# Performance work log

Hardware: AMD Instinct MI355X
Metric: run time of the kernel (lower is better)

## Reference

```python
import jax, jax.numpy as jnp
import numpy as np

N_NODES = 50000
N_EDGES = 800000
F_IN, F_LAT, F_OUT = 64, 64, 64


def _graph_conv(x, W, b, src, dst, deg_out_isqrt, deg_in_isqrt):
    # DGL GraphConv, norm='both': D_out^{-1/2} scaling on src side,
    # linear transform (mult-first since in_feats >= out_feats),
    # scatter-sum to dst, D_in^{-1/2} scaling on dst side, + bias.
    n = x.shape[0]
    h = (x * deg_out_isqrt[:, None]) @ W              # [N, F_out]
    msg = h[src]                                      # [E, F_out] gather
    agg = jax.ops.segment_sum(msg, dst, num_segments=n)  # [N, F_out] scatter
    return agg * deg_in_isqrt[:, None] + b


def setup_inputs() -> dict:
    key = jax.random.key(0)
    ks = jax.random.split(key, 6)
    x = jax.random.normal(ks[0], (N_NODES, F_IN), dtype=jnp.float32)
    W1 = jax.random.normal(ks[1], (F_IN, F_LAT), dtype=jnp.float32) / np.sqrt(F_IN)
    b1 = jnp.zeros((F_LAT,), dtype=jnp.float32)
    W2 = jax.random.normal(ks[2], (F_LAT, F_OUT), dtype=jnp.float32) / np.sqrt(F_LAT)
    b2 = jnp.zeros((F_OUT,), dtype=jnp.float32)
    src = jax.random.randint(ks[3], (N_EDGES,), 0, N_NODES, dtype=jnp.int32)
    dst = jax.random.randint(ks[4], (N_EDGES,), 0, N_NODES, dtype=jnp.int32)
    return {"x": x, "W1": W1, "b1": b1, "W2": W2, "b2": b2, "src": src, "dst": dst}


def reference(x, W1, b1, W2, b2, src, dst):
    n = x.shape[0]
    ones = jnp.ones((src.shape[0],), dtype=x.dtype)
    deg_out = jax.ops.segment_sum(ones, src, num_segments=n)
    deg_in = jax.ops.segment_sum(ones, dst, num_segments=n)
    deg_out_isqrt = jnp.where(deg_out > 0, jax.lax.rsqrt(jnp.maximum(deg_out, 1.0)), 0.0)
    deg_in_isqrt = jnp.where(deg_in > 0, jax.lax.rsqrt(jnp.maximum(deg_in, 1.0)), 0.0)
    h = _graph_conv(x, W1, b1, src, dst, deg_out_isqrt, deg_in_isqrt)
    h = jax.nn.relu(h)
    out = _graph_conv(h, W2, b2, src, dst, deg_out_isqrt, deg_in_isqrt)
    return out
```

## Files before the change

kernel.cpp:

```cpp
#include <hip/hip_runtime.h>

#define NF 64
#define BC 32
#define RANGE 16384
#define RWORDS (RANGE / 4)
#define RANGE2 16384
#define PSPLIT 4

typedef __attribute__((ext_vector_type(8))) short short8;
typedef __attribute__((ext_vector_type(4))) float floatx4;

__device__ __forceinline__ unsigned short f2bf(float f) {
  unsigned int u = __float_as_uint(f);
  return (unsigned short)((u + 0x7fffu + ((u >> 16) & 1u)) >> 16);
}

__global__ __launch_bounds__(512) void hist_kernel(
    const int* __restrict__ src, const int* __restrict__ dst,
    unsigned char* __restrict__ Gout, unsigned char* __restrict__ Gin,
    unsigned char* __restrict__ rank, int n, int nE, int R, int chunk) {
  __shared__ int cnt[RWORDS];
  const int rb = blockIdx.x % (R * BC);
  const int kind = blockIdx.x / (R * BC);
  const int r = rb / BC, b = rb % BC;
  const int r0 = r * RANGE;
  for (int i = threadIdx.x; i < RWORDS; i += 512) cnt[i] = 0;
  __syncthreads();
  const int lo = b * chunk, hi = min(lo + chunk, nE);
  const int* keys = kind ? src : dst;
  const int n4 = (hi > lo) ? ((hi - lo) >> 2) : 0;
  const int4* keys4 = (const int4*)(keys + lo);
  if (kind == 0) {
    for (int i = threadIdx.x; i < n4; i += 512) {
      int4 v = keys4[i];
      int e0 = lo + 4 * i;
      unsigned int k, old, sh;
      k = (unsigned int)(v.x - r0);
      if (k < (unsigned int)RANGE) { sh = (k & 3) * 8; old = atomicAdd(&cnt[k >> 2], 1u << sh); rank[e0 + 0] = (unsigned char)(old >> sh); }
      k = (unsigned int)(v.y - r0);
      if (k < (unsigned int)RANGE) { sh = (k & 3) * 8; old = atomicAdd(&cnt[k >> 2], 1u << sh); rank[e0 + 1] = (unsigned char)(old >> sh); }
      k = (unsigned int)(v.z - r0);
      if (k < (unsigned int)RANGE) { sh = (k & 3) * 8; old = atomicAdd(&cnt[k >> 2], 1u << sh); rank[e0 + 2] = (unsigned char)(old >> sh); }
      k = (unsigned int)(v.w - r0);
      if (k < (unsigned int)RANGE) { sh = (k & 3) * 8; old = atomicAdd(&cnt[k >> 2], 1u << sh); rank[e0 + 3] = (unsigned char)(old >> sh); }
    }
    for (int e = lo + 4 * n4 + threadIdx.x; e < hi; e += 512) {
      unsigned int k = (unsigned int)(keys[e] - r0);
      if (k < (unsigned int)RANGE) {
        unsigned int sh = (k & 3) * 8;
        unsigned int old = atomicAdd(&cnt[k >> 2], 1u << sh);
        rank[e] = (unsigned char)(old >> sh);
      }
    }
    __syncthreads();
    unsigned int* Gw = (unsigned int*)(Gin + (size_t)b * n + r0);
    for (int i = threadIdx.x; i < RWORDS; i += 512)
      if (r0 + 4 * i < n) Gw[i] = (unsigned int)cnt[i];
  } else {
    for (int i = threadIdx.x; i < n4; i += 512) {
      int4 v = keys4[i];
      unsigned int k;
      k = (unsigned int)(v.x - r0);
      if (k < (unsigned int)RANGE) atomicAdd(&cnt[k >> 2], 1u << ((k & 3) * 8));
      k = (unsigned int)(v.y - r0);
      if (k < (unsigned int)RANGE) atomicAdd(&cnt[k >> 2], 1u << ((k & 3) * 8));
      k = (unsigned int)(v.z - r0);
      if (k < (unsigned int)RANGE) atomicAdd(&cnt[k >> 2], 1u << ((k & 3) * 8));
      k = (unsigned int)(v.w - r0);
      if (k < (unsigned int)RANGE) atomicAdd(&cnt[k >> 2], 1u << ((k & 3) * 8));
    }
    for (int e = lo + 4 * n4 + threadIdx.x; e < hi; e += 512) {
      unsigned int k = (unsigned int)(keys[e] - r0);
      if (k < (unsigned int)RANGE) atomicAdd(&cnt[k >> 2], 1u << ((k & 3) * 8));
    }
    __syncthreads();
    unsigned int* Gw = (unsigned int*)(Gout + (size_t)b * n + r0);
    for (int i = threadIdx.x; i < RWORDS; i += 512)
      if (r0 + 4 * i < n) Gw[i] = (unsigned int)cnt[i];
  }
}

__global__ __launch_bounds__(256) void colscan_scan1_kernel(
    unsigned char* __restrict__ Gin, const unsigned char* __restrict__ Gout,
    float* __restrict__ so, float* __restrict__ si,
    int* __restrict__ lscan, int* __restrict__ bsum, int n) {
  __shared__ int s[256];
  const int tid = threadIdx.x;
  const int i = blockIdx.x * 256 + tid;
  int di = 0;
  if (i < n) {
    int base = 0;
    #pragma unroll 8
    for (int b = 0; b < BC; ++b) {
      int c = Gin[(size_t)b * n + i];
      Gin[(size_t)b * n + i] = (unsigned char)base;
      base += c;
    }
    di = base;
    int dsum = 0;
    #pragma unroll 8
    for (int b = 0; b < BC; ++b) dsum += Gout[(size_t)b * n + i];
    si[i] = di > 0 ? rsqrtf((float)di) : 0.f;
    so[i] = dsum > 0 ? rsqrtf((float)dsum) : 0.f;
  }
  s[tid] = di;
  __syncthreads();
  #pragma unroll
  for (int off = 1; off < 256; off <<= 1) {
    int t2 = (tid >= off) ? s[tid - off] : 0;
    __syncthreads();
    s[tid] += t2;
    __syncthreads();
  }
  if (i < n) lscan[i] = s[tid] - di;
  if (tid == 255) bsum[blockIdx.x] = s[255];
}

__global__ __launch_bounds__(256) void scan3_kernel(
    const int* __restrict__ lscan, const int* __restrict__ bsum,
    int* __restrict__ row_start, int n, int nE) {
  __shared__ int red[256];
  const int tid = threadIdx.x;
  const int b = blockIdx.x;
  red[tid] = (tid < b) ? bsum[tid] : 0;
  __syncthreads();
  #pragma unroll
  for (int s = 128; s > 0; s >>= 1) {
    if (tid < s) red[tid] += red[tid + s];
    __syncthreads();
  }
  const int off = red[0];
  const int i = b * 256 + tid;
  if (b == 0 && tid == 0) row_start[n] = nE;
  if (i < n) row_start[i] = lscan[i] + off;
}

__device__ __forceinline__ void mfma_gemm_core(
    const unsigned short* __restrict__ Ab, const unsigned short* __restrict__ Wt,
    unsigned short* __restrict__ H, int row0, int n, int t) {
  const int w = t >> 6, lane = t & 63;
  const int quad = lane >> 4, l15 = lane & 15;
  const short8 a0 = *(const short8*)&Ab[(w * 16 + l15) * 72 + quad * 8];
  const short8 a1 = *(const short8*)&Ab[(w * 16 + l15) * 72 + 32 + quad * 8];
  #pragma unroll
  for (int cg = 0; cg < 4; ++cg) {
    const short8 b0 = *(const short8*)&Wt[(cg * 16 + l15) * 72 + quad * 8];
    const short8 b1 = *(const short8*)&Wt[(cg * 16 + l15) * 72 + 32 + quad * 8];
    floatx4 acc = {0.f, 0.f, 0.f, 0.f};
    acc = __builtin_amdgcn_mfma_f32_16x16x32_bf16(a0, b0, acc, 0, 0, 0);
    acc = __builtin_amdgcn_mfma_f32_16x16x32_bf16(a1, b1, acc, 0, 0, 0);
    #pragma unroll
    for (int reg = 0; reg < 4; ++reg) {
      int grow = row0 + w * 16 + quad * 4 + reg;
      if (grow < n) H[(size_t)grow * NF + cg * 16 + l15] = f2bf(acc[reg]);
    }
  }
}

__device__ __forceinline__ void stage_wt512(
    const float* __restrict__ W, unsigned short* __restrict__ Wt, int t) {
  #pragma unroll
  for (int i = 0; i < 8; ++i) {
    int idx = t + 512 * i;
    int k = idx >> 6, j = idx & 63;
    Wt[j * 72 + k] = f2bf(W[idx]);
  }
}

__global__ __launch_bounds__(512) void place_gemm1_kernel(
    const float* __restrict__ A, const float* __restrict__ so,
    const float* __restrict__ W, unsigned short* __restrict__ H, int n, int ggrid,
    const int* __restrict__ src, const int* __restrict__ dst,
    const unsigned char* __restrict__ rank, const int* __restrict__ row_start,
    const unsigned char* __restrict__ Gin,
    unsigned short* __restrict__ sorted, int nE, int chunk) {
  __shared__ __align__(16) char smem[RANGE2 * 4];
  const int t = threadIdx.x;
  if ((int)blockIdx.x >= ggrid) {
    int* posb = (int*)smem;
    const int pb = blockIdx.x - ggrid;
    const int r = pb / (BC * PSPLIT);
    const int rem = pb % (BC * PSPLIT);
    const int b = rem / PSPLIT;
    const int s = rem % PSPLIT;
    const int r0 = r * RANGE2;
    const int lim = min(RANGE2, n - r0);
    {
      const int4* rs4 = (const int4*)(row_start + r0);
      const unsigned int* g4 = (const unsigned int*)(Gin + (size_t)b * n + r0);
      int4* posb4 = (int4*)posb;
      const int lim4 = lim >> 2;
      for (int i = t; i < lim4; i += 512) {
        int4 rs = rs4[i];
        unsigned int gg = g4[i];
        int4 o;
        o.x = rs.x + (int)(gg & 0xffu);
        o.y = rs.y + (int)((gg >> 8) & 0xffu);
        o.z = rs.z + (int)((gg >> 16) & 0xffu);
        o.w = rs.w + (int)(gg >> 24);
        posb4[i] = o;
      }
    }
    __syncthreads();
    const int lo = b * chunk, hi = min(lo + chunk, nE);
    const int n4 = (hi > lo) ? ((hi - lo) >> 2) : 0;
    const int4* dst4 = (const int4*)(dst + lo);
    const int4* src4 = (const int4*)(src + lo);
    const unsigned int* rank4 = (const unsigned int*)(rank + lo);
    for (int i = t + s * 512; i < n4; i += 512 * PSPLIT) {
      int4 dv = dst4[i];
      int4 sv = src4[i];
      unsigned int rv = rank4[i];
      unsigned int k;
      k = (unsigned int)(dv.x - r0);
      if (k < (unsigned int)lim) sorted[posb[k] + (int)(rv & 0xffu)] = (unsigned short)sv.x;
      k = (unsigned int)(dv.y - r0);
      if (k < (unsigned int)lim) sorted[posb[k] + (int)((rv >> 8) & 0xffu)] = (unsigned short)sv.y;
      k = (unsigned int)(dv.z - r0);
      if (k < (unsigned int)lim) sorted[posb[k] + (int)((rv >> 16) & 0xffu)] = (unsigned short)sv.z;
      k = (unsigned int)(dv.w - r0);
      if (k < (unsigned int)lim) sorted[posb[k] + (int)(rv >> 24)] = (unsigned short)sv.w;
    }
    if (s == 0) {
      for (int e = lo + 4 * n4 + t; e < hi; e += 512) {
        unsigned int k = (unsigned int)(dst[e] - r0);
        if (k < (unsigned int)lim)
          sorted[posb[k] + (int)rank[e]] = (unsigned short)src[e];
      }
    }
    return;
  }
  unsigned short* Ab = (unsigned short*)smem;
  unsigned short* Wt = (unsigned short*)(smem + 128 * 72 * 2);
  stage_wt512(W, Wt, t);
  const int row0 = blockIdx.x * 128;
  #pragma unroll
  for (int i = 0; i < 4; ++i) {
    int idx = t + 512 * i;
    int r = idx >> 4, c4 = idx & 15;
    int gr = row0 + r;
    float4 v = {0.f, 0.f, 0.f, 0.f};
    float sc = 0.f;
    if (gr < n) {
      v = *(const float4*)&A[(size_t)gr * NF + c4 * 4];
      sc = so[gr];
    }
    ushort4 o;
    o.x = f2bf(v.x * sc); o.y = f2bf(v.y * sc);
    o.z = f2bf(v.z * sc); o.w = f2bf(v.w * sc);
    *(ushort4*)&Ab[r * 72 + c4 * 4] = o;
  }
  __syncthreads();
  const int wid = t >> 6;
  const int half = wid >> 2;
  mfma_gemm_core(Ab + half * 64 * 72, Wt, H, row0 + half * 64, n,
                 (wid & 3) * 64 + (t & 63));
}

__device__ __forceinline__ void gather_sum(
    const unsigned short* __restrict__ H, const unsigned short* __restrict__ srcs,
    int beg, int end, int g, int c, float* acc) {
  const float4* Hv = (const float4*)H;
  int e = beg;
  for (; e + 16 <= end; e += 16) {
    int ia = srcs[e + g];
    int ib = srcs[e + 8 + g];
    float4 va = Hv[(size_t)ia * 8 + c];
    float4 vb = Hv[(size_t)ib * 8 + c];
    const unsigned int* pa = (const unsigned int*)&va;
    const unsigned int* pb = (const unsigned int*)&vb;
    #pragma unroll
    for (int k = 0; k < 4; ++k) {
      acc[2 * k]     += __uint_as_float(pa[k] << 16) + __uint_as_float(pb[k] << 16);
      acc[2 * k + 1] += __uint_as_float(pa[k] & 0xffff0000u) + __uint_as_float(pb[k] & 0xffff0000u);
    }
  }
  if (e + 8 <= end) {
    int ia = srcs[e + g];
    float4 va = Hv[(size_t)ia * 8 + c];
    const unsigned int* pa = (const unsigned int*)&va;
    #pragma unroll
    for (int k = 0; k < 4; ++k) {
      acc[2 * k]     += __uint_as_float(pa[k] << 16);
      acc[2 * k + 1] += __uint_as_float(pa[k] & 0xffff0000u);
    }
    e += 8;
  }
  if (e < end) {
    int idx = (e + g < end) ? (e + g) : (end - 1);
    float m = (e + g < end) ? 1.f : 0.f;
    int ia = srcs[idx];
    float4 va = Hv[(size_t)ia * 8 + c];
    const unsigned int* pa = (const unsigned int*)&va;
    #pragma unroll
    for (int k = 0; k < 4; ++k) {
      acc[2 * k]     += m * __uint_as_float(pa[k] << 16);
      acc[2 * k + 1] += m * __uint_as_float(pa[k] & 0xffff0000u);
    }
  }
  #pragma unroll
  for (int d = 8; d <= 32; d <<= 1) {
    #pragma unroll
    for (int k = 0; k < 8; ++k) acc[k] += __shfl_xor(acc[k], d);
  }
}

__global__ __launch_bounds__(256) void agg1_kernel(
    const unsigned short* __restrict__ H1, const int* __restrict__ row_start,
    const unsigned short* __restrict__ srcs, const float* __restrict__ si,
    const float* __restrict__ so, const float* __restrict__ b1,
    unsigned short* __restrict__ T, int n) {
  int node = blockIdx.x * 4 + (threadIdx.x >> 6);
  if (node >= n) return;
  const int lane = threadIdx.x & 63;
  const int g = lane >> 3;
  const int c = lane & 7;
  float acc[8] = {0, 0, 0, 0, 0, 0, 0, 0};
  gather_sum(H1, srcs, row_start[node], row_start[node + 1], g, c, acc);
  if (g == 0) {
    const float sin = si[node];
    const float son = so[node];
    ushort4 o0, o1;
    float v;
    v = fmaxf(fmaf(acc[0], sin, b1[c * 8 + 0]), 0.f) * son; o0.x = f2bf(v);
    v = fmaxf(fmaf(acc[1], sin, b1[c * 8 + 1]), 0.f) * son; o0.y = f2bf(v);
    v = fmaxf(fmaf(acc[2], sin, b1[c * 8 + 2]), 0.f) * son; o0.z = f2bf(v);
    v = fmaxf(fmaf(acc[3], sin, b1[c * 8 + 3]), 0.f) * son; o0.w = f2bf(v);
    v = fmaxf(fmaf(acc[4], sin, b1[c * 8 + 4]), 0.f) * son; o1.x = f2bf(v);
    v = fmaxf(fmaf(acc[5], sin, b1[c * 8 + 5]), 0.f) * son; o1.y = f2bf(v);
    v = fmaxf(fmaf(acc[6], sin, b1[c * 8 + 6]), 0.f) * son; o1.z = f2bf(v);
    v = fmaxf(fmaf(acc[7], sin, b1[c * 8 + 7]), 0.f) * son; o1.w = f2bf(v);
    *(ushort4*)&T[(size_t)node * NF + c * 8]     = o0;
    *(ushort4*)&T[(size_t)node * NF + c * 8 + 4] = o1;
  }
}

__global__ __launch_bounds__(256) void agg2_kernel(
    const unsigned short* __restrict__ Tb, const int* __restrict__ row_start,
    const unsigned short* __restrict__ srcs, const float* __restrict__ si,
    const float* __restrict__ W2, const float* __restrict__ b2,
    float* __restrict__ out, int n) {
  __shared__ __align__(16) float W2s[64 * 64];
  __shared__ float u[4][64];
  const int t = threadIdx.x;
  #pragma unroll
  for (int i = 0; i < 4; ++i)
    *(float4*)&W2s[t * 4 + 1024 * i] = *(const float4*)&W2[t * 4 + 1024 * i];
  const int w = t >> 6;
  const int lane = t & 63;
  const int g = lane >> 3;
  const int c = lane & 7;
  const int node = blockIdx.x * 4 + w;
  const bool valid = node < n;
  float acc[8] = {0, 0, 0, 0, 0, 0, 0, 0};
  if (valid) gather_sum(Tb, srcs, row_start[node], row_start[node + 1], g, c, acc);
  if (g == 0) {
    const float sin = valid ? si[node] : 0.f;
    #pragma unroll
    for (int k = 0; k < 8; ++k) u[w][c * 8 + k] = acc[k] * sin;
  }
  __syncthreads();
  if (valid) {
    float r = b2[lane];
    #pragma unroll
    for (int k = 0; k < 64; ++k) r = fmaf(u[w][k], W2s[k * 64 + lane], r);
    out[(size_t)node * NF + lane] = r;
  }
}

extern "C" void kernel_launch(void* const* d_in, const int* in_sizes, int n_in,
                              void* d_out, int out_size, void* d_ws, size_t ws_size,
                              hipStream_t stream) {
  const float* x  = (const float*)d_in[0];
  const float* W1 = (const float*)d_in[1];
  const float* b1 = (const float*)d_in[2];
  const float* W2 = (const float*)d_in[3];
  const float* b2 = (const float*)d_in[4];
  const int* src  = (const int*)d_in[5];
  const int* dst  = (const int*)d_in[6];
  float* out = (float*)d_out;

  const int N = in_sizes[0] / NF;
  const int E = in_sizes[5];
  const int NB = (N + 255) / 256;
  const int R  = (N + RANGE - 1) / RANGE;
  const int R2 = (N + RANGE2 - 1) / RANGE2;
  const int CH = (((E + BC - 1) / BC) + 3) & ~3;
  (void)ws_size;

  char* ws = (char*)d_ws;
  size_t p = 0;
  auto alloc = [&](size_t bytes) -> void* {
    void* r = ws + p;
    p = (p + bytes + 255) & ~(size_t)255;
    return r;
  };
  float* so         = (float*)alloc((size_t)N * 4);
  float* si         = (float*)alloc((size_t)N * 4);
  int*   row_start  = (int*)  alloc((size_t)(N + 1) * 4);
  int*   bsum       = (int*)  alloc((size_t)NB * 4);
  int*   lscan      = (int*)  alloc((size_t)N * 4);
  unsigned short* sorted_u16 = (unsigned short*)alloc((size_t)E * 2);
  unsigned char*  rank  = (unsigned char*)alloc((size_t)E);
  unsigned short* h1    = (unsigned short*)alloc((size_t)N * NF * 2);
  unsigned char*  G_in  = (unsigned char*)alloc((size_t)BC * N);
  unsigned char*  G_out = (unsigned char*)alloc((size_t)BC * N);
  unsigned short* tb    = (unsigned short*)alloc((size_t)N * NF * 2);

  hist_kernel<<<2 * R * BC, 512, 0, stream>>>(src, dst, G_out, G_in, rank,
                                              N, E, R, CH);

  colscan_scan1_kernel<<<NB, 256, 0, stream>>>(G_in, G_out, so, si,
                                               lscan, bsum, N);

  scan3_kernel<<<NB, 256, 0, stream>>>(lscan, bsum, row_start, N, E);

  const int ggrid = (N + 127) / 128;
  const int pgrid = R2 * BC * PSPLIT;
  const int agrid = (N + 3) / 4;

  place_gemm1_kernel<<<ggrid + pgrid, 512, 0, stream>>>(
      x, so, W1, h1, N, ggrid, src, dst, rank, row_start, G_in,
      sorted_u16, E, CH);

  agg1_kernel<<<agrid, 256, 0, stream>>>(h1, row_start, sorted_u16, si, so, b1, tb, N);

  agg2_kernel<<<agrid, 256, 0, stream>>>(tb, row_start, sorted_u16, si, W2, b2, out, N);
}
```

Baseline: 169.6 us.

## Drop rank array, fuse scan into place, move GEMM1 into aggregation

```diff
diff --git a/kernel.cpp b/kernel.cpp
--- a/kernel.cpp
+++ b/kernel.cpp
@@ -1,14 +1,12 @@
 #include <hip/hip_runtime.h>
 
 #define NF 64
-#define BC 32
+#define BC 64
 #define RANGE 16384
 #define RWORDS (RANGE / 4)
 #define RANGE2 16384
-#define PSPLIT 4
 
 typedef __attribute__((ext_vector_type(8))) short short8;
-typedef __attribute__((ext_vector_type(4))) float floatx4;
 
 __device__ __forceinline__ unsigned short f2bf(float f) {
   unsigned int u = __float_as_uint(f);
@@ -18,7 +16,7 @@
 __global__ __launch_bounds__(512) void hist_kernel(
     const int* __restrict__ src, const int* __restrict__ dst,
     unsigned char* __restrict__ Gout, unsigned char* __restrict__ Gin,
-    unsigned char* __restrict__ rank, int n, int nE, int R, int chunk) {
+    int n, int nE, int R, int chunk) {
   __shared__ int cnt[RWORDS];
   const int rb = blockIdx.x % (R * BC);
   const int kind = blockIdx.x / (R * BC);
@@ -30,64 +28,40 @@
   const int* keys = kind ? src : dst;
   const int n4 = (hi > lo) ? ((hi - lo) >> 2) : 0;
   const int4* keys4 = (const int4*)(keys + lo);
-  if (kind == 0) {
-    for (int i = threadIdx.x; i < n4; i += 512) {
-      int4 v = keys4[i];
-      int e0 = lo + 4 * i;
-      unsigned int k, old, sh;
-      k = (unsigned int)(v.x - r0);
-      if (k < (unsigned int)RANGE) { sh = (k & 3) * 8; old = atomicAdd(&cnt[k >> 2], 1u << sh); rank[e0 + 0] = (unsigned char)(old >> sh); }
-      k = (unsigned int)(v.y - r0);
-      if (k < (unsigned int)RANGE) { sh = (k & 3) * 8; old = atomicAdd(&cnt[k >> 2], 1u << sh); rank[e0 + 1] = (unsigned char)(old >> sh); }
-      k = (unsigned int)(v.z - r0);
-      if (k < (unsigned int)RANGE) { sh = (k & 3) * 8; old = atomicAdd(&cnt[k >> 2], 1u << sh); rank[e0 + 2] = (unsigned char)(old >> sh); }
-      k = (unsigned int)(v.w - r0);
-      if (k < (unsigned int)RANGE) { sh = (k & 3) * 8; old = atomicAdd(&cnt[k >> 2], 1u << sh); rank[e0 + 3] = (unsigned char)(old >> sh); }
-    }
-    for (int e = lo + 4 * n4 + threadIdx.x; e < hi; e += 512) {
-      unsigned int k = (unsigned int)(keys[e] - r0);
-      if (k < (unsigned int)RANGE) {
-        unsigned int sh = (k & 3) * 8;
-        unsigned int old = atomicAdd(&cnt[k >> 2], 1u << sh);
-        rank[e] = (unsigned char)(old >> sh);
-      }
-    }
-    __syncthreads();
-    unsigned int* Gw = (unsigned int*)(Gin + (size_t)b * n + r0);
-    for (int i = threadIdx.x; i < RWORDS; i += 512)
-      if (r0 + 4 * i < n) Gw[i] = (unsigned int)cnt[i];
-  } else {
-    for (int i = threadIdx.x; i < n4; i += 512) {
-      int4 v = keys4[i];
-      unsigned int k;
-      k = (unsigned int)(v.x - r0);
-      if (k < (unsigned int)RANGE) atomicAdd(&cnt[k >> 2], 1u << ((k & 3) * 8));
-      k = (unsigned int)(v.y - r0);
-      if (k < (unsigned int)RANGE) atomicAdd(&cnt[k >> 2], 1u << ((k & 3) * 8));
-      k = (unsigned int)(v.z - r0);
-      if (k < (unsigned int)RANGE) atomicAdd(&cnt[k >> 2], 1u << ((k & 3) * 8));
-      k = (unsigned int)(v.w - r0);
-      if (k < (unsigned int)RANGE) atomicAdd(&cnt[k >> 2], 1u << ((k & 3) * 8));
-    }
-    for (int e = lo + 4 * n4 + threadIdx.x; e < hi; e += 512) {
-      unsigned int k = (unsigned int)(keys[e] - r0);
-      if (k < (unsigned int)RANGE) atomicAdd(&cnt[k >> 2], 1u << ((k & 3) * 8));
-    }
-    __syncthreads();
-    unsigned int* Gw = (unsigned int*)(Gout + (size_t)b * n + r0);
-    for (int i = threadIdx.x; i < RWORDS; i += 512)
-      if (r0 + 4 * i < n) Gw[i] = (unsigned int)cnt[i];
-  }
-}
-
-__global__ __launch_bounds__(256) void colscan_scan1_kernel(
+  for (int i = threadIdx.x; i < n4; i += 512) {
+    int4 v = keys4[i];
+    unsigned int k;
+    k = (unsigned int)(v.x - r0);
+    if (k < (unsigned int)RANGE) atomicAdd(&cnt[k >> 2], 1u << ((k & 3) * 8));
+    k = (unsigned int)(v.y - r0);
+    if (k < (unsigned int)RANGE) atomicAdd(&cnt[k >> 2], 1u << ((k & 3) * 8));
+    k = (unsigned int)(v.z - r0);
+    if (k < (unsigned int)RANGE) atomicAdd(&cnt[k >> 2], 1u << ((k & 3) * 8));
+    k = (unsigned int)(v.w - r0);
+    if (k < (unsigned int)RANGE) atomicAdd(&cnt[k >> 2], 1u << ((k & 3) * 8));
+  }
+  for (int e = lo + 4 * n4 + threadIdx.x; e < hi; e += 512) {
+    unsigned int k = (unsigned int)(keys[e] - r0);
+    if (k < (unsigned int)RANGE) atomicAdd(&cnt[k >> 2], 1u << ((k & 3) * 8));
+  }
+  __syncthreads();
+  unsigned char* G = kind ? Gout : Gin;
+  unsigned int* Gw = (unsigned int*)(G + (size_t)b * n + r0);
+  for (int i = threadIdx.x; i < RWORDS; i += 512)
+    if (r0 + 4 * i < n) Gw[i] = (unsigned int)cnt[i];
+}
+
+__global__ __launch_bounds__(256) void colscan_kernel(
     unsigned char* __restrict__ Gin, const unsigned char* __restrict__ Gout,
+    const float* __restrict__ x, unsigned short* __restrict__ xb,
     float* __restrict__ so, float* __restrict__ si,
     int* __restrict__ lscan, int* __restrict__ bsum, int n) {
   __shared__ int s[256];
+  __shared__ float sos[256];
   const int tid = threadIdx.x;
   const int i = blockIdx.x * 256 + tid;
   int di = 0;
+  float so_v = 0.f;
   if (i < n) {
     int base = 0;
     #pragma unroll 8
@@ -101,8 +75,10 @@
     #pragma unroll 8
     for (int b = 0; b < BC; ++b) dsum += Gout[(size_t)b * n + i];
     si[i] = di > 0 ? rsqrtf((float)di) : 0.f;
-    so[i] = dsum > 0 ? rsqrtf((float)dsum) : 0.f;
-  }
+    so_v = dsum > 0 ? rsqrtf((float)dsum) : 0.f;
+    so[i] = so_v;
+  }
+  sos[tid] = so_v;
   s[tid] = di;
   __syncthreads();
   #pragma unroll
@@ -114,147 +90,92 @@
   }
   if (i < n) lscan[i] = s[tid] - di;
   if (tid == 255) bsum[blockIdx.x] = s[255];
-}
-
-__global__ __launch_bounds__(256) void scan3_kernel(
+  const size_t base4 = (size_t)blockIdx.x * 256 * (NF / 4);
+  const float4* xv = (const float4*)x;
+  #pragma unroll
+  for (int j = 0; j < 16; ++j) {
+    int ci = tid + 256 * j;
+    int nl = ci >> 4;
+    if (blockIdx.x * 256 + nl < n) {
+      float4 v = xv[base4 + ci];
+      float sc = sos[nl];
+      ushort4 o;
+      o.x = f2bf(v.x * sc); o.y = f2bf(v.y * sc);
+      o.z = f2bf(v.z * sc); o.w = f2bf(v.w * sc);
+      *(ushort4*)&xb[(base4 + ci) * 4] = o;
+    }
+  }
+}
+
+__global__ __launch_bounds__(512) void place_kernel(
+    const int* __restrict__ src, const int* __restrict__ dst,
     const int* __restrict__ lscan, const int* __restrict__ bsum,
-    int* __restrict__ row_start, int n, int nE) {
-  __shared__ int red[256];
-  const int tid = threadIdx.x;
-  const int b = blockIdx.x;
-  red[tid] = (tid < b) ? bsum[tid] : 0;
-  __syncthreads();
-  #pragma unroll
-  for (int s = 128; s > 0; s >>= 1) {
-    if (tid < s) red[tid] += red[tid + s];
+    const unsigned char* __restrict__ Gin, int* __restrict__ row_start,
+    unsigned short* __restrict__ sorted, int n, int nE, int nb, int chunk) {
+  __shared__ int posb[RANGE2];
+  __shared__ int offs[256];
+  const int t = threadIdx.x;
+  const int r = blockIdx.x / BC, b = blockIdx.x % BC;
+  const int r0 = r * RANGE2;
+  const int lim = min(RANGE2, n - r0);
+  if (t < 256) offs[t] = (t < nb) ? bsum[t] : 0;
+  __syncthreads();
+  #pragma unroll
+  for (int off = 1; off < 256; off <<= 1) {
+    int v = 0;
+    if (t < 256 && t >= off) v = offs[t - off];
     __syncthreads();
-  }
-  const int off = red[0];
-  const int i = b * 256 + tid;
-  if (b == 0 && tid == 0) row_start[n] = nE;
-  if (i < n) row_start[i] = lscan[i] + off;
-}
-
-__device__ __forceinline__ void mfma_gemm_core(
-    const unsigned short* __restrict__ Ab, const unsigned short* __restrict__ Wt,
-    unsigned short* __restrict__ H, int row0, int n, int t) {
-  const int w = t >> 6, lane = t & 63;
-  const int quad = lane >> 4, l15 = lane & 15;
-  const short8 a0 = *(const short8*)&Ab[(w * 16 + l15) * 72 + quad * 8];
-  const short8 a1 = *(const short8*)&Ab[(w * 16 + l15) * 72 + 32 + quad * 8];
-  #pragma unroll
-  for (int cg = 0; cg < 4; ++cg) {
-    const short8 b0 = *(const short8*)&Wt[(cg * 16 + l15) * 72 + quad * 8];
-    const short8 b1 = *(const short8*)&Wt[(cg * 16 + l15) * 72 + 32 + quad * 8];
-    floatx4 acc = {0.f, 0.f, 0.f, 0.f};
-    acc = __builtin_amdgcn_mfma_f32_16x16x32_bf16(a0, b0, acc, 0, 0, 0);
-    acc = __builtin_amdgcn_mfma_f32_16x16x32_bf16(a1, b1, acc, 0, 0, 0);
-    #pragma unroll
-    for (int reg = 0; reg < 4; ++reg) {
-      int grow = row0 + w * 16 + quad * 4 + reg;
-      if (grow < n) H[(size_t)grow * NF + cg * 16 + l15] = f2bf(acc[reg]);
-    }
-  }
-}
-
-__device__ __forceinline__ void stage_wt512(
-    const float* __restrict__ W, unsigned short* __restrict__ Wt, int t) {
-  #pragma unroll
-  for (int i = 0; i < 8; ++i) {
-    int idx = t + 512 * i;
-    int k = idx >> 6, j = idx & 63;
-    Wt[j * 72 + k] = f2bf(W[idx]);
-  }
-}
-
-__global__ __launch_bounds__(512) void place_gemm1_kernel(
-    const float* __restrict__ A, const float* __restrict__ so,
-    const float* __restrict__ W, unsigned short* __restrict__ H, int n, int ggrid,
-    const int* __restrict__ src, const int* __restrict__ dst,
-    const unsigned char* __restrict__ rank, const int* __restrict__ row_start,
-    const unsigned char* __restrict__ Gin,
-    unsigned short* __restrict__ sorted, int nE, int chunk) {
-  __shared__ __align__(16) char smem[RANGE2 * 4];
-  const int t = threadIdx.x;
-  if ((int)blockIdx.x >= ggrid) {
-    int* posb = (int*)smem;
-    const int pb = blockIdx.x - ggrid;
-    const int r = pb / (BC * PSPLIT);
-    const int rem = pb % (BC * PSPLIT);
-    const int b = rem / PSPLIT;
-    const int s = rem % PSPLIT;
-    const int r0 = r * RANGE2;
-    const int lim = min(RANGE2, n - r0);
-    {
-      const int4* rs4 = (const int4*)(row_start + r0);
-      const unsigned int* g4 = (const unsigned int*)(Gin + (size_t)b * n + r0);
-      int4* posb4 = (int4*)posb;
-      const int lim4 = lim >> 2;
-      for (int i = t; i < lim4; i += 512) {
-        int4 rs = rs4[i];
-        unsigned int gg = g4[i];
-        int4 o;
-        o.x = rs.x + (int)(gg & 0xffu);
-        o.y = rs.y + (int)((gg >> 8) & 0xffu);
-        o.z = rs.z + (int)((gg >> 16) & 0xffu);
-        o.w = rs.w + (int)(gg >> 24);
-        posb4[i] = o;
-      }
-    }
+    if (t < 256) offs[t] += v;
     __syncthreads();
-    const int lo = b * chunk, hi = min(lo + chunk, nE);
-    const int n4 = (hi > lo) ? ((hi - lo) >> 2) : 0;
-    const int4* dst4 = (const int4*)(dst + lo);
-    const int4* src4 = (const int4*)(src + lo);
-    const unsigned int* rank4 = (const unsigned int*)(rank + lo);
-    for (int i = t + s * 512; i < n4; i += 512 * PSPLIT) {
-      int4 dv = dst4[i];
-      int4 sv = src4[i];
-      unsigned int rv = rank4[i];
-      unsigned int k;
-      k = (unsigned int)(dv.x - r0);
-      if (k < (unsigned int)lim) sorted[posb[k] + (int)(rv & 0xffu)] = (unsigned short)sv.x;
-      k = (unsigned int)(dv.y - r0);
-      if (k < (unsigned int)lim) sorted[posb[k] + (int)((rv >> 8) & 0xffu)] = (unsigned short)sv.y;
-      k = (unsigned int)(dv.z - r0);
-      if (k < (unsigned int)lim) sorted[posb[k] + (int)((rv >> 16) & 0xffu)] = (unsigned short)sv.z;
-      k = (unsigned int)(dv.w - r0);
-      if (k < (unsigned int)lim) sorted[posb[k] + (int)(rv >> 24)] = (unsigned short)sv.w;
-    }
-    if (s == 0) {
-      for (int e = lo + 4 * n4 + t; e < hi; e += 512) {
-        unsigned int k = (unsigned int)(dst[e] - r0);
-        if (k < (unsigned int)lim)
-          sorted[posb[k] + (int)rank[e]] = (unsigned short)src[e];
-      }
-    }
-    return;
-  }
-  unsigned short* Ab = (unsigned short*)smem;
-  unsigned short* Wt = (unsigned short*)(smem + 128 * 72 * 2);
-  stage_wt512(W, Wt, t);
-  const int row0 = blockIdx.x * 128;
-  #pragma unroll
-  for (int i = 0; i < 4; ++i) {
-    int idx = t + 512 * i;
-    int r = idx >> 4, c4 = idx & 15;
-    int gr = row0 + r;
-    float4 v = {0.f, 0.f, 0.f, 0.f};
-    float sc = 0.f;
-    if (gr < n) {
-      v = *(const float4*)&A[(size_t)gr * NF + c4 * 4];
-      sc = so[gr];
-    }
-    ushort4 o;
-    o.x = f2bf(v.x * sc); o.y = f2bf(v.y * sc);
-    o.z = f2bf(v.z * sc); o.w = f2bf(v.w * sc);
-    *(ushort4*)&Ab[r * 72 + c4 * 4] = o;
-  }
-  __syncthreads();
-  const int wid = t >> 6;
-  const int half = wid >> 2;
-  mfma_gemm_core(Ab + half * 64 * 72, Wt, H, row0 + half * 64, n,
-                 (wid & 3) * 64 + (t & 63));
+  }
+  {
+    const int4* ls4 = (const int4*)(lscan + r0);
+    const unsigned int* g4 = (const unsigned int*)(Gin + (size_t)b * n + r0);
+    const int lim4 = lim >> 2;
+    for (int i = t; i < lim4; i += 512) {
+      int gi0 = r0 + 4 * i;
+      int j = gi0 >> 8;
+      int off = (j > 0) ? offs[j - 1] : 0;
+      int4 ls = ls4[i];
+      unsigned int gg = g4[i];
+      int4 rs;
+      rs.x = ls.x + off; rs.y = ls.y + off;
+      rs.z = ls.z + off; rs.w = ls.w + off;
+      int4 o;
+      o.x = rs.x + (int)(gg & 0xffu);
+      o.y = rs.y + (int)((gg >> 8) & 0xffu);
+      o.z = rs.z + (int)((gg >> 16) & 0xffu);
+      o.w = rs.w + (int)(gg >> 24);
+      *(int4*)&posb[4 * i] = o;
+      if (b == 0) *(int4*)&row_start[gi0] = rs;
+    }
+  }
+  if (b == 0 && r == 0 && t == 0) row_start[n] = nE;
+  __syncthreads();
+  const int lo = b * chunk, hi = min(lo + chunk, nE);
+  const int n4 = (hi > lo) ? ((hi - lo) >> 2) : 0;
+  const int4* dst4 = (const int4*)(dst + lo);
+  const int4* src4 = (const int4*)(src + lo);
+  for (int i = t; i < n4; i += 512) {
+    int4 dv = dst4[i];
+    int4 sv = src4[i];
+    unsigned int k;
+    k = (unsigned int)(dv.x - r0);
+    if (k < (unsigned int)lim) { int p = atomicAdd(&posb[k], 1); sorted[p] = (unsigned short)sv.x; }
+    k = (unsigned int)(dv.y - r0);
+    if (k < (unsigned int)lim) { int p = atomicAdd(&posb[k], 1); sorted[p] = (unsigned short)sv.y; }
+    k = (unsigned int)(dv.z - r0);
+    if (k < (unsigned int)lim) { int p = atomicAdd(&posb[k], 1); sorted[p] = (unsigned short)sv.z; }
+    k = (unsigned int)(dv.w - r0);
+    if (k < (unsigned int)lim) { int p = atomicAdd(&posb[k], 1); sorted[p] = (unsigned short)sv.w; }
+  }
+  for (int e = lo + 4 * n4 + t; e < hi; e += 512) {
+    unsigned int k = (unsigned int)(dst[e] - r0);
+    if (k < (unsigned int)lim) {
+      int p = atomicAdd(&posb[k], 1);
+      sorted[p] = (unsigned short)src[e];
+    }
+  }
 }
 
 __device__ __forceinline__ void gather_sum(
@@ -306,32 +227,35 @@
 }
 
 __global__ __launch_bounds__(256) void agg1_kernel(
-    const unsigned short* __restrict__ H1, const int* __restrict__ row_start,
+    const unsigned short* __restrict__ Xb, const int* __restrict__ row_start,
     const unsigned short* __restrict__ srcs, const float* __restrict__ si,
-    const float* __restrict__ so, const float* __restrict__ b1,
-    unsigned short* __restrict__ T, int n) {
-  int node = blockIdx.x * 4 + (threadIdx.x >> 6);
-  if (node >= n) return;
-  const int lane = threadIdx.x & 63;
+    const float* __restrict__ so, const float* __restrict__ W1,
+    const float* __restrict__ b1, unsigned short* __restrict__ T, int n) {
+  __shared__ __align__(16) float Ws[64 * 64];
+  __shared__ float u[4][64];
+  const int t = threadIdx.x;
+  #pragma unroll
+  for (int i = 0; i < 4; ++i)
+    *(float4*)&Ws[t * 4 + 1024 * i] = *(const float4*)&W1[t * 4 + 1024 * i];
+  const int w = t >> 6;
+  const int lane = t & 63;
   const int g = lane >> 3;
   const int c = lane & 7;
+  const int node = blockIdx.x * 4 + w;
+  const bool valid = node < n;
   float acc[8] = {0, 0, 0, 0, 0, 0, 0, 0};
-  gather_sum(H1, srcs, row_start[node], row_start[node + 1], g, c, acc);
+  if (valid) gather_sum(Xb, srcs, row_start[node], row_start[node + 1], g, c, acc);
   if (g == 0) {
-    const float sin = si[node];
-    const float son = so[node];
-    ushort4 o0, o1;
-    float v;
-    v = fmaxf(fmaf(acc[0], sin, b1[c * 8 + 0]), 0.f) * son; o0.x = f2bf(v);
-    v = fmaxf(fmaf(acc[1], sin, b1[c * 8 + 1]), 0.f) * son; o0.y = f2bf(v);
-    v = fmaxf(fmaf(acc[2], sin, b1[c * 8 + 2]), 0.f) * son; o0.z = f2bf(v);
-    v = fmaxf(fmaf(acc[3], sin, b1[c * 8 + 3]), 0.f) * son; o0.w = f2bf(v);
-    v = fmaxf(fmaf(acc[4], sin, b1[c * 8 + 4]), 0.f) * son; o1.x = f2bf(v);
-    v = fmaxf(fmaf(acc[5], sin, b1[c * 8 + 5]), 0.f) * son; o1.y = f2bf(v);
-    v = fmaxf(fmaf(acc[6], sin, b1[c * 8 + 6]), 0.f) * son; o1.z = f2bf(v);
-    v = fmaxf(fmaf(acc[7], sin, b1[c * 8 + 7]), 0.f) * son; o1.w = f2bf(v);
-    *(ushort4*)&T[(size_t)node * NF + c * 8]     = o0;
-    *(ushort4*)&T[(size_t)node * NF + c * 8 + 4] = o1;
+    #pragma unroll
+    for (int k = 0; k < 8; ++k) u[w][c * 8 + k] = acc[k];
+  }
+  __syncthreads();
+  if (valid) {
+    float r = 0.f;
+    #pragma unroll
+    for (int k = 0; k < 64; ++k) r = fmaf(u[w][k], Ws[k * 64 + lane], r);
+    float v = fmaxf(fmaf(r, si[node], b1[lane]), 0.f) * so[node];
+    T[(size_t)node * NF + lane] = f2bf(v);
   }
 }
 
@@ -401,29 +325,24 @@
   int*   bsum       = (int*)  alloc((size_t)NB * 4);
   int*   lscan      = (int*)  alloc((size_t)N * 4);
   unsigned short* sorted_u16 = (unsigned short*)alloc((size_t)E * 2);
-  unsigned char*  rank  = (unsigned char*)alloc((size_t)E);
-  unsigned short* h1    = (unsigned short*)alloc((size_t)N * NF * 2);
+  unsigned short* xb    = (unsigned short*)alloc((size_t)N * NF * 2);
   unsigned char*  G_in  = (unsigned char*)alloc((size_t)BC * N);
   unsigned char*  G_out = (unsigned char*)alloc((size_t)BC * N);
   unsigned short* tb    = (unsigned short*)alloc((size_t)N * NF * 2);
 
-  hist_kernel<<<2 * R * BC, 512, 0, stream>>>(src, dst, G_out, G_in, rank,
-                                              N, E, R, CH);
-
-  colscan_scan1_kernel<<<NB, 256, 0, stream>>>(G_in, G_out, so, si,
-                                               lscan, bsum, N);
-
-  scan3_kernel<<<NB, 256, 0, stream>>>(lscan, bsum, row_start, N, E);
-
-  const int ggrid = (N + 127) / 128;
-  const int pgrid = R2 * BC * PSPLIT;
+  hist_kernel<<<2 * R * BC, 512, 0, stream>>>(src, dst, G_out, G_in, N, E, R, CH);
+
+  colscan_kernel<<<NB, 256, 0, stream>>>(G_in, G_out, x, xb, so, si,
+                                         lscan, bsum, N);
+
+  place_kernel<<<R2 * BC, 512, 0, stream>>>(src, dst, lscan, bsum, G_in,
+                                            row_start, sorted_u16, N, E, NB, CH);
+
   const int agrid = (N + 3) / 4;
 
-  place_gemm1_kernel<<<ggrid + pgrid, 512, 0, stream>>>(
-      x, so, W1, h1, N, ggrid, src, dst, rank, row_start, G_in,
-      sorted_u16, E, CH);
-
-  agg1_kernel<<<agrid, 256, 0, stream>>>(h1, row_start, sorted_u16, si, so, b1, tb, N);
-
-  agg2_kernel<<<agrid, 256, 0, stream>>>(tb, row_start, sorted_u16, si, W2, b2, out, N);
-}
+  agg1_kernel<<<agrid, 256, 0, stream>>>(xb, row_start, sorted_u16, si, so,
+                                         W1, b1, tb, N);
+
+  agg2_kernel<<<agrid, 256, 0, stream>>>(tb, row_start, sorted_u16, si,
+                                         W2, b2, out, N);
+}
```

New measurement: 193.5 us. 1.14x slower.
